# Kernel optimization log

Measured on AMD Instinct MI355X. Metric: run time of the kernel, lower is better.

Reference implementation:

```python
import jax, jax.numpy as jnp
import numpy as np

N = 100000
E = 1600000
IN_C = 128
HID = 256
EPS = 1e-5


def setup_inputs() -> dict:
    key = jax.random.key(0)
    ks = jax.random.split(key, 20)
    s = lambda fi, fo: (1.0 / np.sqrt(fi))
    inp = {
        "x": jax.random.normal(ks[0], (N, IN_C), dtype=jnp.float32),
        "edge_index": jax.random.randint(ks[1], (2, E), 0, N, dtype=jnp.int64),
        # SAGEConv (in -> hidden): lin_l (on aggregated neighbors, with bias), lin_r (root, no bias)
        "Wl": jax.random.normal(ks[2], (HID, IN_C), dtype=jnp.float32) * s(IN_C, HID),
        "bl": jnp.zeros((HID,), dtype=jnp.float32),
        "Wr": jax.random.normal(ks[3], (HID, IN_C), dtype=jnp.float32) * s(IN_C, HID),
        # bns[0]
        "bn_g": jnp.ones((HID,), dtype=jnp.float32),
        "bn_b": jnp.zeros((HID,), dtype=jnp.float32),
        # linear stack hidden->hidden->64->14->2
        "W1": jax.random.normal(ks[4], (HID, HID), dtype=jnp.float32) * s(HID, HID),
        "b1": jnp.zeros((HID,), dtype=jnp.float32),
        "W2": jax.random.normal(ks[5], (64, HID), dtype=jnp.float32) * s(HID, 64),
        "b2": jnp.zeros((64,), dtype=jnp.float32),
        "W3": jax.random.normal(ks[6], (14, 64), dtype=jnp.float32) * s(64, 14),
        "b3": jnp.zeros((14,), dtype=jnp.float32),
        "W4": jax.random.normal(ks[7], (2, 14), dtype=jnp.float32) * s(14, 2),
        "b4": jnp.zeros((2,), dtype=jnp.float32),
        # bns2: BN(hidden), BN(64), BN(14)
        "g1": jnp.ones((HID,), dtype=jnp.float32), "bb1": jnp.zeros((HID,), dtype=jnp.float32),
        "g2": jnp.ones((64,), dtype=jnp.float32), "bb2": jnp.zeros((64,), dtype=jnp.float32),
        "g3": jnp.ones((14,), dtype=jnp.float32), "bb3": jnp.zeros((14,), dtype=jnp.float32),
    }
    return inp


def _bn(h, g, b):
    # training-mode BatchNorm1d: batch mean, biased variance
    m = h.mean(axis=0)
    v = jnp.mean((h - m) ** 2, axis=0)
    return g * (h - m) * jax.lax.rsqrt(v + EPS) + b


def _sage_mean(x, edge_index, Wl, bl, Wr):
    src, dst = edge_index[0], edge_index[1]
    n = x.shape[0]
    agg = jax.ops.segment_sum(x[src], dst, num_segments=n)  # [N, F]
    cnt = jax.ops.segment_sum(jnp.ones((src.shape[0],), x.dtype), dst, num_segments=n)
    agg = agg / jnp.maximum(cnt, 1.0)[:, None]
    return agg @ Wl.T + bl + x @ Wr.T


def reference(x, edge_index, Wl, bl, Wr, bn_g, bn_b,
              W1, b1, W2, b2, W3, b3, W4, b4,
              g1, bb1, g2, bb2, g3, bb3):
    # convs2[:-1] loop (num_layers=2 -> single conv), dropout is identity (eval)
    h = _sage_mean(x, edge_index, Wl, bl, Wr)
    h = jax.nn.relu(_bn(h, bn_g, bn_b))
    # linear stack with bns2 + relu
    h = jax.nn.relu(_bn(h @ W1.T + b1, g1, bb1))
    h = jax.nn.relu(_bn(h @ W2.T + b2, g2, bb2))
    h = jax.nn.relu(_bn(h @ W3.T + b3, g3, bb3))
    h = h @ W4.T + b4
    return jax.nn.log_softmax(h, axis=-1)
```

## Files before the change

### kernel.cpp

```cpp
#include <hip/hip_runtime.h>
#include <math.h>

#define BN_EPS 1e-5f
#define STAT_NB 64
#define GBIN 512
#define BSH 7

typedef unsigned short u16;
typedef __attribute__((ext_vector_type(8))) unsigned short u16x8;
typedef __attribute__((ext_vector_type(8))) short bf16x8;
typedef __attribute__((ext_vector_type(4))) float f32x4;

__device__ __forceinline__ float bf2f(u16 b){
  union{unsigned int u; float f;} c; c.u = ((unsigned int)b)<<16; return c.f;
}
__device__ __forceinline__ u16 f2bf(float f){
  union{float f; unsigned int u;} c; c.f=f;
  unsigned int u = c.u;
  return (u16)((u + 0x7fffu + ((u>>16)&1u)) >> 16);
}

__global__ __launch_bounds__(256) void k_prep(
    const float* __restrict__ Wl, const float* __restrict__ Wr,
    const float* __restrict__ W1, const float* __restrict__ W2,
    const float* __restrict__ x,
    u16* __restrict__ Wb1, u16* __restrict__ Wb2, u16* __restrict__ Wb3,
    u16* __restrict__ Acat, int n, int* __restrict__ flags){
  int bid = blockIdx.x, tid = threadIdx.x;
  if (bid==0 && tid<8) flags[tid]=0;
  auto cv8 = [](const float* s)->u16x8{
    float4 a = ((const float4*)s)[0], b = ((const float4*)s)[1];
    u16x8 v;
    v[0]=f2bf(a.x); v[1]=f2bf(a.y); v[2]=f2bf(a.z); v[3]=f2bf(a.w);
    v[4]=f2bf(b.x); v[5]=f2bf(b.y); v[6]=f2bf(b.z); v[7]=f2bf(b.w);
    return v;
  };
  if (bid < 32){
    int i = bid*256 + tid;
    int c = i>>5, kb = (i&31)*8;
    const float* src = (kb<128) ? (Wl + (size_t)c*128 + kb) : (Wr + (size_t)c*128 + kb-128);
    *(u16x8*)(Wb1 + (size_t)c*256 + kb) = cv8(src);
  } else if (bid < 64){
    int i = (bid-32)*256 + tid;
    *(u16x8*)(Wb2 + (size_t)i*8) = cv8(W1 + (size_t)i*8);
  } else if (bid < 72){
    int i = (bid-64)*256 + tid;
    if (i < 2048) *(u16x8*)(Wb3 + (size_t)i*8) = cv8(W2 + (size_t)i*8);
  } else {
    int i = (bid-72)*256 + tid;
    int total = n*16;
    int stride = (gridDim.x-72)*256;
    for (; i<total; i+=stride){
      int r = i>>4, kb = (i&15)*8;
      *(u16x8*)(Acat + (size_t)r*256 + 128 + kb) = cv8(x + (size_t)r*128 + kb);
    }
  }
}


__global__ __launch_bounds__(256) void k_hist(const int* __restrict__ ei, int E, int nbkt,
                                              int* __restrict__ blkhist){
  __shared__ int hist[1024];
  int tid = threadIdx.x, blk = blockIdx.x;
  for (int b=tid;b<1024;b+=256) hist[b]=0;
  __syncthreads();
  int per = (E + GBIN - 1)/GBIN;
  int e0 = blk*per, e1 = min(E, e0+per);
  for (int e=e0+tid; e<e1; e+=256)
    atomicAdd(&hist[ei[(size_t)E+e]>>BSH], 1);
  __syncthreads();
  for (int b=tid;b<nbkt;b+=256) blkhist[(size_t)blk*nbkt + b] = hist[b];
}

__global__ void k_rowscan(int* __restrict__ blkhist, int nbkt, int* __restrict__ bbase){
  int b = blockIdx.x*blockDim.x + threadIdx.x;
  if (b >= nbkt) return;
  int run = 0;
  for (int k=0;k<GBIN;k++){
    size_t idx = (size_t)k*nbkt + b;
    int t = blkhist[idx];
    blkhist[idx] = run;
    run += t;
  }
  bbase[b] = run;
}

__global__ void k_bscan(int* __restrict__ bbase, int nbkt){
  __shared__ int s[1024];
  int tid = threadIdx.x;
  int v = (tid<nbkt)? bbase[tid] : 0;
  s[tid]=v; __syncthreads();
  #pragma unroll
  for (int o=1;o<1024;o<<=1){
    int t = (tid>=o)? s[tid-o] : 0;
    __syncthreads();
    s[tid]+=t;
    __syncthreads();
  }
  if (tid<nbkt) bbase[tid] = s[tid]-v;
  if (tid==1023) bbase[nbkt] = s[1023];
}

__global__ __launch_bounds__(256) void k_scatter(const int* __restrict__ ei, int E, int nbkt,
                                                 const int* __restrict__ blkhist,
                                                 const int* __restrict__ bbase,
                                                 int* __restrict__ pairs){
  __shared__ int cur[1024];
  int tid = threadIdx.x, blk = blockIdx.x;
  for (int b=tid;b<nbkt;b+=256) cur[b] = bbase[b] + blkhist[(size_t)blk*nbkt + b];
  __syncthreads();
  int per = (E + GBIN - 1)/GBIN;
  int e0 = blk*per, e1 = min(E, e0+per);
  for (int e=e0+tid; e<e1; e+=256){
    int dst = ei[(size_t)E+e];
    int src = ei[e];
    int b = dst>>BSH;
    int p = atomicAdd(&cur[b], 1);
    pairs[p] = (src<<BSH) | (dst & 127);
  }
}

__global__ __launch_bounds__(256) void k_bucket_csr(const int* __restrict__ pairs,
                                                    const int* __restrict__ bbase,
                                                    int nbkt, int n,
                                                    int* __restrict__ deg, int* __restrict__ off,
                                                    int* __restrict__ eidx){
  __shared__ int hist[128], loff[128], cur2[128];
  int tid = threadIdx.x, b = blockIdx.x;
  if (b >= nbkt) return;
  int n0 = b<<BSH;
  int nn = min(128, n - n0);
  int e0 = bbase[b], e1 = bbase[b+1];
  int cnt = e1 - e0;
  if (tid<128) hist[tid]=0;
  __syncthreads();
  for (int i=tid;i<cnt;i+=256)
    atomicAdd(&hist[pairs[e0+i] & 127], 1);
  __syncthreads();
  int hv=0;
  if (tid<128){ hv = hist[tid]; loff[tid] = hv; }
  __syncthreads();
  #pragma unroll
  for (int o=1;o<128;o<<=1){
    int t = (tid<128 && tid>=o)? loff[tid-o] : 0;
    __syncthreads();
    if (tid<128) loff[tid]+=t;
    __syncthreads();
  }
  if (tid<128){
    int ex = loff[tid]-hv;
    cur2[tid] = ex;
    if (tid<nn){
      deg[n0+tid] = hv;
      off[n0+tid] = e0 + ex;
    }
  }
  __syncthreads();
  for (int i=tid;i<cnt;i+=256){
    int v = pairs[e0+i];
    int p = atomicAdd(&cur2[v & 127], 1);
    eidx[e0 + p] = v>>BSH;
  }
}

__global__ void k_aggregate(u16* Acat, const int* __restrict__ off,
                            const int* __restrict__ deg, const int* __restrict__ eidx, int n){
  int wid = (blockIdx.x*blockDim.x + threadIdx.x) >> 6;
  int lane = threadIdx.x & 63;
  if (wid >= n) return;
  int o = off[wid], d = deg[wid];
  int eslot = lane >> 3;
  int ck = (lane & 7) * 16;
  float f[16];
  #pragma unroll
  for (int j=0;j<16;j++) f[j]=0.f;
  #pragma unroll 2
  for (int i = eslot; i < d; i += 8){
    int s = eidx[o+i];
    const u16x8* src = (const u16x8*)(Acat + (size_t)s*256 + 128 + ck);
    u16x8 v0 = src[0], v1 = src[1];
    #pragma unroll
    for (int j=0;j<8;j++) f[j]   += bf2f(v0[j]);
    #pragma unroll
    for (int j=0;j<8;j++) f[8+j] += bf2f(v1[j]);
  }
  #pragma unroll
  for (int j=0;j<16;j++){
    f[j] += __shfl_xor(f[j], 8, 64);
    f[j] += __shfl_xor(f[j], 16, 64);
    f[j] += __shfl_xor(f[j], 32, 64);
  }
  if (lane < 8){
    float inv = 1.f/(float)max(d,1);
    u16x8 r0, r1;
    #pragma unroll
    for (int j=0;j<8;j++){ r0[j]=f2bf(f[j]*inv); r1[j]=f2bf(f[8+j]*inv); }
    u16x8* dst = (u16x8*)(Acat + (size_t)wid*256 + ck);
    dst[0]=r0; dst[1]=r1;
  }
}


template<int COLS>
__global__ __launch_bounds__(256, 2) void k_gemm_mfma(
    const u16* __restrict__ A, const u16* __restrict__ W,
    const float* __restrict__ ss, int has_ss,
    const float* __restrict__ bias, u16* __restrict__ out,
    int nrows, int hout,
    float* __restrict__ psum, float* __restrict__ psq)
{
  constexpr int WN  = COLS/2;
  constexpr int NFR = WN/16;
  __shared__ u16 As[128*64];
  __shared__ u16 Bs[COLS*64];
  __shared__ float scs[256], shs[256];
  __shared__ float red[2][2][COLS];

  int tid  = threadIdx.x;
  int lane = tid & 63, wave = tid >> 6;
  int wr = wave >> 1, wc = wave & 1;
  int rbase = blockIdx.x*128;
  constexpr int cbase = 0;

  if (has_ss){ scs[tid] = ss[tid]; shs[tid] = ss[256+tid]; }
  __syncthreads();

  f32x4 acc[4][NFR];
  #pragma unroll
  for (int m=0;m<4;m++)
    #pragma unroll
    for (int n=0;n<NFR;n++)
      acc[m][n] = (f32x4){0.f,0.f,0.f,0.f};

  int arow = tid >> 1;
  int acb  = (tid & 1) * 32;
  bool avalid = (rbase + arow) < nrows;
  const u16* aptr = A + (size_t)(rbase+arow)*256 + acb;
  int brow, bcb;
  if (COLS==256)      { brow = tid;    bcb = 0; }
  else if (COLS==128) { brow = tid>>1; bcb = (tid&1)*32; }
  else                { brow = tid>>2; bcb = (tid&3)*16; }
  const u16* bptr = W + (size_t)(cbase+brow)*256 + bcb;

  for (int kt=0; kt<256; kt+=64){
    #pragma unroll
    for (int q=0;q<4;q++){
      u16x8 v = (u16x8){0,0,0,0,0,0,0,0};
      if (avalid) v = *(const u16x8*)(aptr + kt + q*8);
      if (has_ss){
        int k = acb + q*8;
        #pragma unroll
        for (int e=0;e<8;e++){
          float f = bf2f(v[e]);
          f = fmaxf(fmaf(f, scs[kt+k+e], shs[kt+k+e]), 0.f);
          v[e] = f2bf(f);
        }
      }
      int slot = ((acb>>3) + q) ^ (arow & 7);
      *(u16x8*)(As + arow*64 + slot*8) = v;
    }
    #pragma unroll
    for (int q=0;q<(COLS==256?8:COLS/32);q++){
      u16x8 v = *(const u16x8*)(bptr + kt + q*8);
      int slot = ((bcb>>3) + q) ^ (brow & 7);
      *(u16x8*)(Bs + brow*64 + slot*8) = v;
    }
    __syncthreads();

    int fr = lane & 15, g = lane >> 4;
    #pragma unroll
    for (int kk=0;kk<2;kk++){
      bf16x8 af[4], bfr[NFR];
      #pragma unroll
      for (int m=0;m<4;m++){
        int row = wr*64 + m*16 + fr;
        int slot = (kk*4 + g) ^ (row & 7);
        af[m] = *(const bf16x8*)(As + row*64 + slot*8);
      }
      #pragma unroll
      for (int n=0;n<NFR;n++){
        int row = wc*WN + n*16 + fr;
        int slot = (kk*4 + g) ^ (row & 7);
        bfr[n] = *(const bf16x8*)(Bs + row*64 + slot*8);
      }
      #pragma unroll
      for (int m=0;m<4;m++)
        #pragma unroll
        for (int n=0;n<NFR;n++)
          acc[m][n] = __builtin_amdgcn_mfma_f32_16x16x32_bf16(af[m], bfr[n], acc[m][n], 0, 0, 0);
    }
    __syncthreads();
  }

  int cl = lane & 15, g = lane >> 4;
  float bv[NFR], sn[NFR], qn[NFR];
  #pragma unroll
  for (int n=0;n<NFR;n++){
    bv[n] = bias[cbase + wc*WN + n*16 + cl];
    sn[n] = 0.f; qn[n] = 0.f;
  }
  #pragma unroll
  for (int m=0;m<4;m++){
    int r0 = rbase + wr*64 + m*16 + g*4;
    #pragma unroll
    for (int n=0;n<NFR;n++){
      int c = cbase + wc*WN + n*16 + cl;
      #pragma unroll
      for (int i=0;i<4;i++){
        int r = r0 + i;
        if (r < nrows){
          float v = acc[m][n][i] + bv[n];
          out[(size_t)r*hout + c] = f2bf(v);
          sn[n] += v; qn[n] += v*v;
        }
      }
    }
  }
  #pragma unroll
  for (int n=0;n<NFR;n++){
    sn[n] += __shfl_xor(sn[n], 16, 64);
    sn[n] += __shfl_xor(sn[n], 32, 64);
    qn[n] += __shfl_xor(qn[n], 16, 64);
    qn[n] += __shfl_xor(qn[n], 32, 64);
  }
  if (lane < 16){
    #pragma unroll
    for (int n=0;n<NFR;n++){
      int cc = wc*WN + n*16 + lane;
      red[0][wr][cc] = sn[n];
      red[1][wr][cc] = qn[n];
    }
  }
  __syncthreads();
  if (tid < COLS){
    psum[(size_t)blockIdx.x*hout + cbase + tid] = red[0][0][tid] + red[0][1][tid];
    psq [(size_t)blockIdx.x*hout + cbase + tid] = red[1][0][tid] + red[1][1][tid];
  }
}

__global__ __launch_bounds__(256) void k_stats_partfold(
    const float* __restrict__ psum, const float* __restrict__ psq,
    int rt, int h, float* __restrict__ part, float ninv,
    const float* __restrict__ g, const float* __restrict__ b_,
    float* __restrict__ ss, int* __restrict__ counter){
  __shared__ int isLast;
  int c = threadIdx.x, b = blockIdx.x;
  int chunk = (rt + STAT_NB - 1)/STAT_NB;
  int i0 = b*chunk;
  int i1 = min(rt, i0+chunk);
  if (c < h){
    float s0=0.f,s1=0.f,s2=0.f,s3=0.f, q0=0.f,q1=0.f,q2=0.f,q3=0.f;
    int i=i0;
    for (; i+3<i1; i+=4){
      s0 += psum[(size_t)i*h+c];     q0 += psq[(size_t)i*h+c];
      s1 += psum[(size_t)(i+1)*h+c]; q1 += psq[(size_t)(i+1)*h+c];
      s2 += psum[(size_t)(i+2)*h+c]; q2 += psq[(size_t)(i+2)*h+c];
      s3 += psum[(size_t)(i+3)*h+c]; q3 += psq[(size_t)(i+3)*h+c];
    }
    for (; i<i1; ++i){ s0 += psum[(size_t)i*h+c]; q0 += psq[(size_t)i*h+c]; }
    part[((size_t)b*2  )*h + c] = (s0+s1)+(s2+s3);
    part[((size_t)b*2+1)*h + c] = (q0+q1)+(q2+q3);
  }
  __threadfence();
  if (c==0) isLast = (atomicAdd(counter,1) == gridDim.x-1);
  __syncthreads();
  if (isLast && c < h){
    float S0=0.f,S1=0.f,Q0=0.f,Q1=0.f;
    #pragma unroll 2
    for (int b2=0;b2<STAT_NB;b2+=2){
      S0 += part[((size_t)b2*2  )*h + c];
      Q0 += part[((size_t)b2*2+1)*h + c];
      S1 += part[((size_t)(b2+1)*2  )*h + c];
      Q1 += part[((size_t)(b2+1)*2+1)*h + c];
    }
    float S = S0+S1, Q = Q0+Q1;
    float m = S*ninv;
    float v = fmaxf(Q*ninv - m*m, 0.f);
    float sc = g[c] * rsqrtf(v + BN_EPS);
    ss[c]   = sc;
    ss[h+c] = b_[c] - m*sc;
  }
}

__global__ __launch_bounds__(256) void k_lin3(const u16* __restrict__ h3, const float* __restrict__ ss3,
     const float* __restrict__ W3, const float* __restrict__ b3,
     float* __restrict__ h4, int n, float* __restrict__ psum, float* __restrict__ psq){
  __shared__ float Ws[14*64];
  __shared__ float bs[14];
  __shared__ float sc[64], sh[64];
  __shared__ float redp[2][14][4];
  int tid=threadIdx.x;
  for (int i=tid;i<896;i+=256) Ws[i]=W3[i];
  if (tid<14) bs[tid]=b3[tid];
  if (tid<64){ sc[tid]=ss3[tid]; sh[tid]=ss3[64+tid]; }
  __syncthreads();
  int node = blockIdx.x*256 + tid;
  float o[14];
  #pragma unroll
  for (int hh=0;hh<14;hh++) o[hh]=0.f;
  if (node<n){
    const u16x8* ar = (const u16x8*)(h3 + (size_t)node*64);
    #pragma unroll
    for (int kv=0;kv<8;kv++){
      u16x8 v = ar[kv];
      #pragma unroll
      for (int j=0;j<8;j++){
        int k=kv*8+j;
        float a = fmaxf(fmaf(bf2f(v[j]), sc[k], sh[k]), 0.f);
        #pragma unroll
        for (int hh=0;hh<14;hh++) o[hh] = fmaf(a, Ws[hh*64+k], o[hh]);
      }
    }
    #pragma unroll
    for (int hh=0;hh<14;hh++){ o[hh]+=bs[hh]; h4[(size_t)node*14+hh]=o[hh]; }
  }
  int lane = tid & 63, w = tid>>6;
  #pragma unroll
  for (int hh=0;hh<14;hh++){
    float sv = (node<n)? o[hh] : 0.f;
    float qv = sv*sv;
    #pragma unroll
    for (int offs=32;offs>0;offs>>=1){
      sv += __shfl_down(sv,offs,64);
      qv += __shfl_down(qv,offs,64);
    }
    if (lane==0){ redp[0][hh][w]=sv; redp[1][hh][w]=qv; }
  }
  __syncthreads();
  if (tid<14){
    float t=redp[0][tid][0]+redp[0][tid][1]+redp[0][tid][2]+redp[0][tid][3];
    psum[(size_t)blockIdx.x*14+tid]=t;
  } else if (tid>=64 && tid<78){
    int c=tid-64;
    float t=redp[1][c][0]+redp[1][c][1]+redp[1][c][2]+redp[1][c][3];
    psq[(size_t)blockIdx.x*14+c]=t;
  }
}

__global__ void k_final(const float* __restrict__ h4, const float* __restrict__ ss4,
   const float* __restrict__ W4, const float* __restrict__ b4, float* __restrict__ out, int n){
  int node = blockIdx.x*blockDim.x+threadIdx.x;
  if (node>=n) return;
  float z0=b4[0], z1=b4[1];
  #pragma unroll
  for (int j=0;j<14;j++){
    float a = fmaxf(h4[(size_t)node*14+j]*ss4[j]+ss4[14+j], 0.f);
    z0 = fmaf(a, W4[j],    z0);
    z1 = fmaf(a, W4[14+j], z1);
  }
  float m = fmaxf(z0,z1);
  float lse = m + logf(expf(z0-m)+expf(z1-m));
  out[(size_t)node*2]   = z0-lse;
  out[(size_t)node*2+1] = z1-lse;
}

extern "C" void kernel_launch(void* const* d_in, const int* in_sizes, int n_in,
                              void* d_out, int out_size, void* d_ws, size_t ws_size,
                              hipStream_t stream){
  const float* x    = (const float*)d_in[0];
  const int*   ei   = (const int*)d_in[1];
  const float* Wl   = (const float*)d_in[2];
  const float* bl   = (const float*)d_in[3];
  const float* Wr   = (const float*)d_in[4];
  const float* bn_g = (const float*)d_in[5];
  const float* bn_b = (const float*)d_in[6];
  const float* W1   = (const float*)d_in[7];
  const float* b1   = (const float*)d_in[8];
  const float* W2   = (const float*)d_in[9];
  const float* b2   = (const float*)d_in[10];
  const float* W3   = (const float*)d_in[11];
  const float* b3   = (const float*)d_in[12];
  const float* W4   = (const float*)d_in[13];
  const float* b4   = (const float*)d_in[14];
  const float* g1   = (const float*)d_in[15];
  const float* bb1  = (const float*)d_in[16];
  const float* g2   = (const float*)d_in[17];
  const float* bb2  = (const float*)d_in[18];
  const float* g3   = (const float*)d_in[19];
  const float* bb3  = (const float*)d_in[20];

  const int N = in_sizes[0]/128;
  const int E = in_sizes[1]/2;
  const int NBKT = (N + 127) >> BSH;
  const int RT2 = (N+127)/128;
  const int RT4 = (N+255)/256;

  char* p = (char*)d_ws;
  auto alloc = [&](size_t bytes)->void*{
    void* r = (void*)p;
    p += (bytes + 255) & ~(size_t)255;
    return r;
  };
  int* deg      = (int*)alloc((size_t)N*sizeof(int));
  int* off      = (int*)alloc((size_t)N*sizeof(int));
  int* bbase    = (int*)alloc(1025*sizeof(int));
  int* flags    = (int*)alloc(16*sizeof(int));
  int* blkhist  = (int*)alloc((size_t)1024*GBIN*sizeof(int));
  int* pairs    = (int*)alloc((size_t)E*sizeof(int));
  int* eidx     = (int*)alloc((size_t)E*sizeof(int));
  u16* Acat     = (u16*)alloc((size_t)N*256*sizeof(u16));
  u16* h1b      = (u16*)alloc((size_t)N*256*sizeof(u16));
  float* h4     = (float*)alloc((size_t)N*14*sizeof(float));
  u16* Wb1      = (u16*)alloc(256*256*sizeof(u16));
  u16* Wb2      = (u16*)alloc(256*256*sizeof(u16));
  u16* Wb3      = (u16*)alloc(64*256*sizeof(u16));
  float* psum   = (float*)alloc((size_t)RT2*256*sizeof(float));
  float* psq    = (float*)alloc((size_t)RT2*256*sizeof(float));
  float* part   = (float*)alloc((size_t)STAT_NB*2*256*sizeof(float));
  float* ssb    = (float*)alloc(4*512*sizeof(float));
  u16* h2b = Acat;
  u16* h3b = h1b;
  float* ss1=ssb, *ss2=ssb+512, *ss3=ssb+1024, *ss4=ssb+1536;
  const float ninv = 1.f/(float)N;

  k_prep<<<dim3(72+2048), dim3(256), 0, stream>>>(Wl, Wr, W1, W2, x, Wb1, Wb2, Wb3, Acat, N, flags);

  k_hist<<<dim3(GBIN), dim3(256), 0, stream>>>(ei, E, NBKT, blkhist);
  k_rowscan<<<dim3((NBKT+255)/256), dim3(256), 0, stream>>>(blkhist, NBKT, bbase);
  k_bscan<<<dim3(1), dim3(1024), 0, stream>>>(bbase, NBKT);
  k_scatter<<<dim3(GBIN), dim3(256), 0, stream>>>(ei, E, NBKT, blkhist, bbase, pairs);
  k_bucket_csr<<<dim3(NBKT), dim3(256), 0, stream>>>(pairs, bbase, NBKT, N, deg, off, eidx);

  k_aggregate<<<dim3((N+3)/4), dim3(256), 0, stream>>>(Acat, off, deg, eidx, N);

  k_gemm_mfma<256><<<dim3(RT2), dim3(256), 0, stream>>>(
      Acat, Wb1, (const float*)0, 0, bl, h1b, N, 256, psum, psq);
  k_stats_partfold<<<dim3(STAT_NB), dim3(256), 0, stream>>>(
      psum, psq, RT2, 256, part, ninv, bn_g, bn_b, ss1, flags+0);

  k_gemm_mfma<256><<<dim3(RT2), dim3(256), 0, stream>>>(
      h1b, Wb2, ss1, 1, b1, h2b, N, 256, psum, psq);
  k_stats_partfold<<<dim3(STAT_NB), dim3(256), 0, stream>>>(
      psum, psq, RT2, 256, part, ninv, g1, bb1, ss2, flags+1);

  k_gemm_mfma<64><<<dim3(RT2), dim3(256), 0, stream>>>(
      h2b, Wb3, ss2, 1, b2, h3b, N, 64, psum, psq);
  k_stats_partfold<<<dim3(STAT_NB), dim3(256), 0, stream>>>(
      psum, psq, RT2, 64, part, ninv, g2, bb2, ss3, flags+2);

  k_lin3<<<dim3(RT4), dim3(256), 0, stream>>>(h3b, ss3, W3, b3, h4, N, psum, psq);
  k_stats_partfold<<<dim3(STAT_NB), dim3(256), 0, stream>>>(
      psum, psq, RT4, 14, part, ninv, g3, bb3, ss4, flags+3);

  k_final<<<dim3((N+255)/256), dim3(256), 0, stream>>>(h4, ss4, W4, b4, (float*)d_out, N);
}
```

Measured before the change: 365.4 us.

## Transpose block histogram and scan each bucket row with one wavefront

The per-block histogram is stored bucket-major instead of block-major. The row scan then gives each bucket a 64-lane wavefront that loads 8 contiguous counts per lane and combines them with a shuffle-based prefix scan. Previously one thread per bucket walked 512 strided entries serially across only a few blocks. The hist and scatter kernels now write and read the histogram with a stride of GBIN, which makes their global accesses less coalesced in exchange.

```diff
diff --git a/kernel.cpp b/kernel.cpp
--- a/kernel.cpp
+++ b/kernel.cpp
@@ -69,20 +69,31 @@
   for (int e=e0+tid; e<e1; e+=256)
     atomicAdd(&hist[ei[(size_t)E+e]>>BSH], 1);
   __syncthreads();
-  for (int b=tid;b<nbkt;b+=256) blkhist[(size_t)blk*nbkt + b] = hist[b];
-}
-
-__global__ void k_rowscan(int* __restrict__ blkhist, int nbkt, int* __restrict__ bbase){
-  int b = blockIdx.x*blockDim.x + threadIdx.x;
-  if (b >= nbkt) return;
-  int run = 0;
-  for (int k=0;k<GBIN;k++){
-    size_t idx = (size_t)k*nbkt + b;
-    int t = blkhist[idx];
-    blkhist[idx] = run;
-    run += t;
-  }
-  bbase[b] = run;
+  for (int b=tid;b<nbkt;b+=256) blkhist[(size_t)b*GBIN + blk] = hist[b];
+}
+
+__global__ __launch_bounds__(256) void k_rowscan(int* __restrict__ blkhist, int nbkt,
+                                                 int* __restrict__ bbase){
+  int wid = (blockIdx.x*blockDim.x + threadIdx.x) >> 6;
+  int lane = threadIdx.x & 63;
+  if (wid >= nbkt) return;
+  int* row = blkhist + (size_t)wid*GBIN + lane*8;
+  int v[8];
+  #pragma unroll
+  for (int j=0;j<8;j++) v[j] = row[j];
+  int s = 0;
+  #pragma unroll
+  for (int j=0;j<8;j++){ int t = v[j]; v[j] = s; s += t; }
+  int incl = s;
+  #pragma unroll
+  for (int o=1;o<64;o<<=1){
+    int t = __shfl_up(incl, o, 64);
+    if (lane >= o) incl += t;
+  }
+  int excl = incl - s;
+  #pragma unroll
+  for (int j=0;j<8;j++) row[j] = v[j] + excl;
+  if (lane == 63) bbase[wid] = incl;
 }
 
 __global__ void k_bscan(int* __restrict__ bbase, int nbkt){
@@ -107,7 +118,7 @@
                                                  int* __restrict__ pairs){
   __shared__ int cur[1024];
   int tid = threadIdx.x, blk = blockIdx.x;
-  for (int b=tid;b<nbkt;b+=256) cur[b] = bbase[b] + blkhist[(size_t)blk*nbkt + b];
+  for (int b=tid;b<nbkt;b+=256) cur[b] = bbase[b] + blkhist[(size_t)b*GBIN + blk];
   __syncthreads();
   int per = (E + GBIN - 1)/GBIN;
   int e0 = blk*per, e1 = min(E, e0+per);
@@ -516,7 +527,7 @@
   k_prep<<<dim3(72+2048), dim3(256), 0, stream>>>(Wl, Wr, W1, W2, x, Wb1, Wb2, Wb3, Acat, N, flags);
 
   k_hist<<<dim3(GBIN), dim3(256), 0, stream>>>(ei, E, NBKT, blkhist);
-  k_rowscan<<<dim3((NBKT+255)/256), dim3(256), 0, stream>>>(blkhist, NBKT, bbase);
+  k_rowscan<<<dim3((NBKT*64+255)/256), dim3(256), 0, stream>>>(blkhist, NBKT, bbase);
   k_bscan<<<dim3(1), dim3(1024), 0, stream>>>(bbase, NBKT);
   k_scatter<<<dim3(GBIN), dim3(256), 0, stream>>>(ei, E, NBKT, blkhist, bbase, pairs);
   k_bucket_csr<<<dim3(NBKT), dim3(256), 0, stream>>>(pairs, bbase, NBKT, N, deg, off, eidx);
```

New measurement: 302.0 us. 1.21x faster.
